# Kernel tuning notes

Hardware: AMD Instinct MI355X
Metric: run time of the kernel (lower is better)

Reference implementation:

```python
import jax, jax.numpy as jnp
import numpy as np

LOC_SIZE, TIM_SIZE = 50000, 48
LOC_EMB, TIM_EMB = 512, 32
IN = LOC_EMB + TIM_EMB  # 544
HID = 1024
SEQ, TGT = 4096, 1024


def _gru(x, Wih, Whh, bih, bhh):
    """PyTorch-convention GRU over [S, IN] -> [S, HID], h0 = 0."""
    gi = x @ Wih.T + bih  # [S, 3H] precomputed input gates
    H = Whh.shape[1]

    def step(h, gi_t):
        gh = Whh @ h + bhh
        i_r, i_z, i_n = jnp.split(gi_t, 3)
        h_r, h_z, h_n = jnp.split(gh, 3)
        r = jax.nn.sigmoid(i_r + h_r)
        z = jax.nn.sigmoid(i_z + h_z)
        n = jnp.tanh(i_n + r * h_n)
        h_new = (1.0 - z) * n + z * h
        return h_new, h_new

    _, hs = jax.lax.scan(step, jnp.zeros((H,), x.dtype), gi)
    return hs


def setup_inputs() -> dict:
    key = jax.random.key(0)
    ks = jax.random.split(key, 16)
    s = 0.02
    inp = {
        "loc": jax.random.randint(ks[0], (SEQ, 1), 0, LOC_SIZE),
        "tim": jax.random.randint(ks[1], (SEQ, 1), 0, TIM_SIZE),
        "target_len": TGT,
        "emb_loc": jax.random.normal(ks[2], (LOC_SIZE, LOC_EMB), jnp.float32) * s,
        "emb_tim": jax.random.normal(ks[3], (TIM_SIZE, TIM_EMB), jnp.float32) * s,
        "Wih_enc": jax.random.normal(ks[4], (3 * HID, IN), jnp.float32) * s,
        "Whh_enc": jax.random.normal(ks[5], (3 * HID, HID), jnp.float32) * s,
        "bih_enc": jnp.zeros((3 * HID,), jnp.float32),
        "bhh_enc": jnp.zeros((3 * HID,), jnp.float32),
        "Wih_dec": jax.random.normal(ks[6], (3 * HID, IN), jnp.float32) * s,
        "Whh_dec": jax.random.normal(ks[7], (3 * HID, HID), jnp.float32) * s,
        "bih_dec": jnp.zeros((3 * HID,), jnp.float32),
        "bhh_dec": jnp.zeros((3 * HID,), jnp.float32),
        "W_fc": jax.random.normal(ks[8], (LOC_SIZE, 2 * HID), jnp.float32) * s,
        "b_fc": jnp.zeros((LOC_SIZE,), jnp.float32),
    }
    return inp


def reference(loc, tim, target_len, emb_loc, emb_tim,
              Wih_enc, Whh_enc, bih_enc, bhh_enc,
              Wih_dec, Whh_dec, bih_dec, bhh_dec,
              W_fc, b_fc):
    # embeddings, batch dim of 1 squeezed: [S, IN]
    x = jnp.concatenate([emb_loc[loc[:, 0]], emb_tim[tim[:, 0]]], axis=1)
    # dropout is identity in eval mode
    hidden_history = _gru(x[:-target_len], Wih_enc, Whh_enc, bih_enc, bhh_enc)  # [S-T, H]
    hidden_state = _gru(x[-target_len:], Wih_dec, Whh_dec, bih_dec, bhh_dec)    # [T, H]
    # 'dot' attention: fused GEMM + row softmax (replaces the O(T*S) python loop)
    energies = hidden_state @ hidden_history.T                                   # [T, S-T]
    attn_weights = jax.nn.softmax(energies, axis=-1)
    context = attn_weights @ hidden_history                                      # [T, H]
    out = jnp.concatenate([hidden_state, context], axis=1)                       # [T, 2H]
    y = out @ W_fc.T + b_fc                                                      # [T, LOC_SIZE]
    return jax.nn.log_softmax(y, axis=-1)
```

## Files before the change

kernel.cpp:

```cpp
#include <hip/hip_runtime.h>
#include <hip/hip_bf16.h>
#include <cstdint>

typedef __attribute__((ext_vector_type(4))) float floatx4;
typedef __attribute__((ext_vector_type(8))) __bf16 bf16x8;
typedef __attribute__((ext_vector_type(4))) __bf16 bf16x4;
typedef unsigned long long u64t;

#define HID    1024
#define SEQ    4096
#define TGT    1024
#define ENC_T  3072
#define IN_DIM 544
#define NCLS   50000

__global__ __launch_bounds__(128) void embed_kernel(
    const int* __restrict__ loc, const int* __restrict__ tim,
    const float* __restrict__ el, const float* __restrict__ et,
    float* __restrict__ x) {
  int row = blockIdx.x, t = threadIdx.x;
  int li = loc[row], ti = tim[row];
  float4 v = *(const float4*)(el + (size_t)li * 512 + t * 4);
  *(float4*)(x + (size_t)row * IN_DIM + t * 4) = v;
  if (t < 8) {
    float4 w = *(const float4*)(et + (size_t)ti * 32 + t * 4);
    *(float4*)(x + (size_t)row * IN_DIM + 512 + t * 4) = w;
  }
}

#define BK  64
#define LDT 72

__global__ __launch_bounds__(256) void gemm_nt(
    const float* __restrict__ A, int lda,
    const float* __restrict__ B, int ldb,
    float* __restrict__ C, int ldc,
    const float* __restrict__ bias,
    int M, int N, int K) {
  __shared__ __bf16 As[128 * LDT];
  __shared__ __bf16 Bs[128 * LDT];
  const int tid = threadIdx.x;
  const int bm = blockIdx.x * 128, bn = blockIdx.y * 128;
  const int wave = tid >> 6, lane = tid & 63;
  const int wm = (wave & 1) * 64, wn = (wave >> 1) * 64;
  const int fr = lane & 15;
  const int kq = (lane >> 4) * 8;

  floatx4 acc[4][4];
#pragma unroll
  for (int i = 0; i < 4; i++)
#pragma unroll
    for (int j = 0; j < 4; j++) acc[i][j] = (floatx4){0.f, 0.f, 0.f, 0.f};

  const int nkt = (K + BK - 1) / BK;
  for (int kt = 0; kt < nkt; ++kt) {
    const int k0 = kt * BK;
#pragma unroll
    for (int i = 0; i < 8; i++) {
      int flat = tid + i * 256;
      int r = flat >> 4;
      int c4 = (flat & 15) * 4;
      float4 va = {0, 0, 0, 0}, vb = {0, 0, 0, 0};
      if (k0 + c4 < K) {
        va = *(const float4*)(A + (size_t)(bm + r) * lda + k0 + c4);
        if (bn + r < N) vb = *(const float4*)(B + (size_t)(bn + r) * ldb + k0 + c4);
      }
      *(bf16x4*)(As + r * LDT + c4) =
          (bf16x4){(__bf16)va.x, (__bf16)va.y, (__bf16)va.z, (__bf16)va.w};
      *(bf16x4*)(Bs + r * LDT + c4) =
          (bf16x4){(__bf16)vb.x, (__bf16)vb.y, (__bf16)vb.z, (__bf16)vb.w};
    }
    __syncthreads();
#pragma unroll
    for (int kh = 0; kh < 2; ++kh) {
      const int kf = kh * 32 + kq;
      bf16x8 af[4], bfr[4];
#pragma unroll
      for (int i = 0; i < 4; i++) {
        af[i]  = *(const bf16x8*)(As + (wm + i * 16 + fr) * LDT + kf);
        bfr[i] = *(const bf16x8*)(Bs + (wn + i * 16 + fr) * LDT + kf);
      }
#pragma unroll
      for (int mi = 0; mi < 4; mi++)
#pragma unroll
        for (int ni = 0; ni < 4; ni++)
          acc[mi][ni] = __builtin_amdgcn_mfma_f32_16x16x32_bf16(
              af[mi], bfr[ni], acc[mi][ni], 0, 0, 0);
    }
    __syncthreads();
  }

  const int em = (lane >> 4) * 4;
#pragma unroll
  for (int mi = 0; mi < 4; mi++) {
#pragma unroll
    for (int ni = 0; ni < 4; ni++) {
      int gn = bn + wn + ni * 16 + fr;
      if (gn < N) {
        float bv = bias ? bias[gn] : 0.f;
        int gm = bm + wm + mi * 16 + em;
#pragma unroll
        for (int r2 = 0; r2 < 4; r2++)
          C[(size_t)(gm + r2) * ldc + gn] = acc[mi][ni][r2] + bv;
      }
    }
  }
}

#define SC_WGS 128

__device__ __forceinline__ float bsel(unsigned int u, int half) {
  return __builtin_bit_cast(float, half ? (u & 0xffff0000u) : (u << 16));
}

__global__ __launch_bounds__(256) void scan_kernel(
    const float* __restrict__ Whh_e, const float* __restrict__ bhh_e, const float* __restrict__ gi_e,
    const float* __restrict__ Whh_d, const float* __restrict__ bhh_d, const float* __restrict__ gi_d,
    float* __restrict__ Hh, float* __restrict__ HhT, float* __restrict__ outcat,
    u64t* __restrict__ hbuf_e, u64t* __restrict__ hbuf_d) {
  const bool enc = blockIdx.x < SC_WGS;
  const int wid = enc ? blockIdx.x : (blockIdx.x - SC_WGS);
  const int T = enc ? ENC_T : TGT;
  const float* Whh = enc ? Whh_e : Whh_d;
  const float* bhh = enc ? bhh_e : bhh_d;
  const float* gi  = enc ? gi_e : gi_d;
  u64t* hbuf = enc ? hbuf_e : hbuf_d;

  __shared__ uint2 wrz[8 * 512];
  __shared__ unsigned int wnn[8 * 512];
  const int tid = threadIdx.x;

  for (int i = tid; i < 8 * 512; i += 256) {
    int el = i >> 9, k2 = i & 511;
    int rb = wid * 8 + el;
    float2 w0 = *(const float2*)(Whh + (size_t)(0 * HID + rb) * HID + 2 * k2);
    float2 w1 = *(const float2*)(Whh + (size_t)(1 * HID + rb) * HID + 2 * k2);
    float2 w2 = *(const float2*)(Whh + (size_t)(2 * HID + rb) * HID + 2 * k2);
    unsigned int p0 = (unsigned int)__builtin_bit_cast(unsigned short, (__bf16)w0.x) |
                      ((unsigned int)__builtin_bit_cast(unsigned short, (__bf16)w0.y) << 16);
    unsigned int p1 = (unsigned int)__builtin_bit_cast(unsigned short, (__bf16)w1.x) |
                      ((unsigned int)__builtin_bit_cast(unsigned short, (__bf16)w1.y) << 16);
    unsigned int p2 = (unsigned int)__builtin_bit_cast(unsigned short, (__bf16)w2.x) |
                      ((unsigned int)__builtin_bit_cast(unsigned short, (__bf16)w2.y) << 16);
    wrz[i] = make_uint2(p0, p1);
    wnn[i] = p2;
  }
  __syncthreads();

  const int l = tid & 63;
  const int w = tid >> 6;
  const int le0 = w * 2, le1 = le0 + 1;
  const int e0 = wid * 8 + le0;
  const int half = l & 1;
  const int kbase = l >> 1;

  float bq = 0.f;
  if (l < 3) bq = bhh[l * HID + e0];
  else if (l >= 4 && l < 7) bq = bhh[(l - 4) * HID + (e0 + 1)];

  long budget = 1L << 21;

  for (int t = 0; t < T; ++t) {
    float gval = 0.f;
    if (l < 3) gval = gi[(size_t)t * 3072 + l * HID + e0];
    else if (l >= 4 && l < 7) gval = gi[(size_t)t * 3072 + (l - 4) * HID + (e0 + 1)];

    const u64t* hp = hbuf + ((t + 1) & 1) * HID;
    float ar0, az0, an0, ar1, az1, an1, hpe = 0.f;
    for (;;) {
      u64t hv[16];
#pragma unroll
      for (int j = 0; j < 16; ++j)
        hv[j] = __hip_atomic_load(hp + l + 64 * j, __ATOMIC_RELAXED, __HIP_MEMORY_SCOPE_AGENT);
      u64t we = 0;
      if (l < 2) we = __hip_atomic_load(hp + e0 + l, __ATOMIC_RELAXED, __HIP_MEMORY_SCOPE_AGENT);
      bool ok = true;
      ar0 = az0 = an0 = ar1 = az1 = an1 = 0.f;
#pragma unroll
      for (int j = 0; j < 16; ++j) {
        ok &= (unsigned int)(hv[j] >> 32) >= (unsigned int)t;
        float h = __builtin_bit_cast(float, (unsigned int)hv[j]);
        int k2 = kbase + 32 * j;
        uint2 u0 = wrz[le0 * 512 + k2];
        unsigned int n0 = wnn[le0 * 512 + k2];
        uint2 u1 = wrz[le1 * 512 + k2];
        unsigned int n1 = wnn[le1 * 512 + k2];
        ar0 += bsel(u0.x, half) * h;
        az0 += bsel(u0.y, half) * h;
        an0 += bsel(n0, half) * h;
        ar1 += bsel(u1.x, half) * h;
        az1 += bsel(u1.y, half) * h;
        an1 += bsel(n1, half) * h;
      }
      if (l < 2) {
        ok &= (unsigned int)(we >> 32) >= (unsigned int)t;
        hpe = __builtin_bit_cast(float, (unsigned int)we);
      }
      if (__all(ok)) break;
      if (--budget < 0) break;
    }
#pragma unroll
    for (int o = 32; o; o >>= 1) {
      ar0 += __shfl_xor(ar0, o); az0 += __shfl_xor(az0, o); an0 += __shfl_xor(an0, o);
      ar1 += __shfl_xor(ar1, o); az1 += __shfl_xor(az1, o); an1 += __shfl_xor(an1, o);
    }
    int base = half * 4;
    float i_r = __shfl(gval, base + 0);
    float i_z = __shfl(gval, base + 1);
    float i_n = __shfl(gval, base + 2);
    float b_r = __shfl(bq, base + 0);
    float b_z = __shfl(bq, base + 1);
    float b_n = __shfl(bq, base + 2);
    __syncthreads();
    if (l < 2) {
      float sr = l ? ar1 : ar0;
      float sz = l ? az1 : az0;
      float sn = l ? an1 : an0;
      int e = e0 + l;
      float r = 1.f / (1.f + expf(-(i_r + sr + b_r)));
      float z = 1.f / (1.f + expf(-(i_z + sz + b_z)));
      float nn2 = tanhf(i_n + r * (sn + b_n));
      float hnew = (1.f - z) * nn2 + z * hpe;
      u64t pk = ((u64t)(unsigned int)(t + 1) << 32) |
                (u64t)__builtin_bit_cast(unsigned int, hnew);
      __hip_atomic_store(&hbuf[(t & 1) * HID + e], pk,
                         __ATOMIC_RELAXED, __HIP_MEMORY_SCOPE_AGENT);
      if (enc) {
        Hh[(size_t)t * HID + e] = hnew;
        HhT[(size_t)e * ENC_T + t] = hnew;
      } else {
        outcat[(size_t)t * 2048 + e] = hnew;
      }
    }
  }
}

__device__ __forceinline__ float wave_max(float v) {
#pragma unroll
  for (int o = 32; o; o >>= 1) v = fmaxf(v, __shfl_xor(v, o));
  return v;
}
__device__ __forceinline__ float wave_sum(float v) {
#pragma unroll
  for (int o = 32; o; o >>= 1) v += __shfl_xor(v, o);
  return v;
}

__global__ __launch_bounds__(256) void softmax_kernel(float* __restrict__ E) {
  __shared__ float red[4];
  int row = blockIdx.x;
  float* p = E + (size_t)row * ENC_T;
  int tid = threadIdx.x, wave = tid >> 6;
  float v[12];
  float m = -3.4e38f;
#pragma unroll
  for (int j = 0; j < 12; j++) { v[j] = p[tid + j * 256]; m = fmaxf(m, v[j]); }
  m = wave_max(m);
  if ((tid & 63) == 0) red[wave] = m;
  __syncthreads();
  m = fmaxf(fmaxf(red[0], red[1]), fmaxf(red[2], red[3]));
  __syncthreads();
  float s = 0.f;
#pragma unroll
  for (int j = 0; j < 12; j++) { v[j] = expf(v[j] - m); s += v[j]; }
  s = wave_sum(s);
  if ((tid & 63) == 0) red[wave] = s;
  __syncthreads();
  s = red[0] + red[1] + red[2] + red[3];
  float inv = 1.f / s;
#pragma unroll
  for (int j = 0; j < 12; j++) p[tid + j * 256] = v[j] * inv;
}

__global__ __launch_bounds__(256) void lse_kernel(const float* __restrict__ Y,
                                                  float* __restrict__ lse) {
  __shared__ float red[4];
  int row = blockIdx.x;
  const float* p = Y + (size_t)row * NCLS;
  int tid = threadIdx.x, wave = tid >> 6;
  float m = -3.4e38f;
  for (int c = tid; c < NCLS; c += 256) m = fmaxf(m, p[c]);
  m = wave_max(m);
  if ((tid & 63) == 0) red[wave] = m;
  __syncthreads();
  m = fmaxf(fmaxf(red[0], red[1]), fmaxf(red[2], red[3]));
  __syncthreads();
  float s = 0.f;
  for (int c = tid; c < NCLS; c += 256) s += expf(p[c] - m);
  s = wave_sum(s);
  if ((tid & 63) == 0) red[wave] = s;
  __syncthreads();
  if (tid == 0) lse[row] = m + logf(red[0] + red[1] + red[2] + red[3]);
}

__global__ __launch_bounds__(256) void sub_kernel(float* __restrict__ Y,
                                                  const float* __restrict__ lse) {
  const unsigned total = (unsigned)TGT * (NCLS / 4);
  unsigned stride = gridDim.x * 256;
  for (unsigned i = blockIdx.x * 256 + threadIdx.x; i < total; i += stride) {
    unsigned row = i / (NCLS / 4);
    float l = lse[row];
    float4 v = ((float4*)Y)[i];
    v.x -= l; v.y -= l; v.z -= l; v.w -= l;
    ((float4*)Y)[i] = v;
  }
}

extern "C" void kernel_launch(void* const* d_in, const int* in_sizes, int n_in,
                              void* d_out, int out_size, void* d_ws, size_t ws_size,
                              hipStream_t stream) {
  const int*   loc     = (const int*)d_in[0];
  const int*   tim     = (const int*)d_in[1];
  const float* emb_loc = (const float*)d_in[3];
  const float* emb_tim = (const float*)d_in[4];
  const float* Wih_e   = (const float*)d_in[5];
  const float* Whh_e   = (const float*)d_in[6];
  const float* bih_e   = (const float*)d_in[7];
  const float* bhh_e   = (const float*)d_in[8];
  const float* Wih_d   = (const float*)d_in[9];
  const float* Whh_d   = (const float*)d_in[10];
  const float* bih_d   = (const float*)d_in[11];
  const float* bhh_d   = (const float*)d_in[12];
  const float* W_fc    = (const float*)d_in[13];
  const float* b_fc    = (const float*)d_in[14];
  float* out = (float*)d_out;

  float* ws = (float*)d_ws;
  u64t* hbuf_e = (u64t*)ws;
  u64t* hbuf_d = (u64t*)(ws + 4096);
  float* lse    = ws + 8192;
  float* x      = ws + 9216;
  float* gi_e   = x + (size_t)SEQ * IN_DIM;
  float* gi_d   = gi_e + (size_t)ENC_T * 3072;
  float* Hh     = gi_d + (size_t)TGT * 3072;
  float* HhT    = Hh + (size_t)ENC_T * HID;
  float* outcat = HhT + (size_t)HID * ENC_T;
  float* energ  = outcat + (size_t)TGT * 2048;

  hipMemsetAsync(d_ws, 0, 8192 * sizeof(float), stream);

  embed_kernel<<<SEQ, 128, 0, stream>>>(loc, tim, emb_loc, emb_tim, x);

  gemm_nt<<<dim3(ENC_T / 128, 3072 / 128), 256, 0, stream>>>(
      x, IN_DIM, Wih_e, IN_DIM, gi_e, 3072, bih_e, ENC_T, 3072, IN_DIM);
  gemm_nt<<<dim3(TGT / 128, 3072 / 128), 256, 0, stream>>>(
      x + (size_t)ENC_T * IN_DIM, IN_DIM, Wih_d, IN_DIM, gi_d, 3072, bih_d, TGT, 3072, IN_DIM);

  scan_kernel<<<2 * SC_WGS, 256, 0, stream>>>(Whh_e, bhh_e, gi_e, Whh_d, bhh_d, gi_d,
                                              Hh, HhT, outcat, hbuf_e, hbuf_d);

  gemm_nt<<<dim3(TGT / 128, ENC_T / 128), 256, 0, stream>>>(
      outcat, 2048, Hh, HID, energ, ENC_T, nullptr, TGT, ENC_T, HID);
  softmax_kernel<<<TGT, 256, 0, stream>>>(energ);
  gemm_nt<<<dim3(TGT / 128, HID / 128), 256, 0, stream>>>(
      energ, ENC_T, HhT, ENC_T, outcat + HID, 2048, nullptr, TGT, HID, ENC_T);

  gemm_nt<<<dim3(TGT / 128, (NCLS + 127) / 128), 256, 0, stream>>>(
      outcat, 2048, W_fc, 2048, out, NCLS, b_fc, TGT, NCLS, 2048);

  lse_kernel<<<TGT, 256, 0, stream>>>(out, lse);
  sub_kernel<<<4096, 256, 0, stream>>>(out, lse);
}
```

Before: 15.11 ms.

## Pack GRU hidden-state exchange as bf16 value plus 16-bit step tag

The cross-workgroup hidden-state buffer now stores each element as a 32-bit word: a bf16 value plus a 16-bit step counter, replacing the 64-bit fp32-plus-tag word. Each lane polls half as many 64-bit atomic words per step, and each word carries two h elements. Each workgroup keeps its own previous h in an fp32 register instead of re-reading it, and the per-step __syncthreads is dropped. The cost is that the recurrent matvec now uses a bf16-rounded h, which may cost accuracy over the long scan.

```diff
diff --git a/kernel.cpp b/kernel.cpp
--- a/kernel.cpp
+++ b/kernel.cpp
@@ -109,22 +109,25 @@
 
 #define SC_WGS 128
 
-__device__ __forceinline__ float bsel(unsigned int u, int half) {
-  return __builtin_bit_cast(float, half ? (u & 0xffff0000u) : (u << 16));
+__device__ __forceinline__ float flo(unsigned int u) {
+  return __builtin_bit_cast(float, u << 16);
+}
+__device__ __forceinline__ float fhi(unsigned int u) {
+  return __builtin_bit_cast(float, u & 0xffff0000u);
 }
 
 __global__ __launch_bounds__(256) void scan_kernel(
     const float* __restrict__ Whh_e, const float* __restrict__ bhh_e, const float* __restrict__ gi_e,
     const float* __restrict__ Whh_d, const float* __restrict__ bhh_d, const float* __restrict__ gi_d,
     float* __restrict__ Hh, float* __restrict__ HhT, float* __restrict__ outcat,
-    u64t* __restrict__ hbuf_e, u64t* __restrict__ hbuf_d) {
+    unsigned int* __restrict__ hbuf_e, unsigned int* __restrict__ hbuf_d) {
   const bool enc = blockIdx.x < SC_WGS;
   const int wid = enc ? blockIdx.x : (blockIdx.x - SC_WGS);
   const int T = enc ? ENC_T : TGT;
   const float* Whh = enc ? Whh_e : Whh_d;
   const float* bhh = enc ? bhh_e : bhh_d;
   const float* gi  = enc ? gi_e : gi_d;
-  u64t* hbuf = enc ? hbuf_e : hbuf_d;
+  unsigned int* hbuf = enc ? hbuf_e : hbuf_d;
 
   __shared__ uint2 wrz[8 * 512];
   __shared__ unsigned int wnn[8 * 512];
@@ -151,13 +154,17 @@
   const int w = tid >> 6;
   const int le0 = w * 2, le1 = le0 + 1;
   const int e0 = wid * 8 + le0;
-  const int half = l & 1;
-  const int kbase = l >> 1;
 
   float bq = 0.f;
   if (l < 3) bq = bhh[l * HID + e0];
   else if (l >= 4 && l < 7) bq = bhh[(l - 4) * HID + (e0 + 1)];
 
+  const uint2* wrz0 = wrz + le0 * 512;
+  const uint2* wrz1 = wrz + le1 * 512;
+  const unsigned int* wnn0 = wnn + le0 * 512;
+  const unsigned int* wnn1 = wnn + le1 * 512;
+
+  float h_own = 0.f;
   long budget = 1L << 21;
 
   for (int t = 0; t < T; ++t) {
@@ -165,36 +172,34 @@
     if (l < 3) gval = gi[(size_t)t * 3072 + l * HID + e0];
     else if (l >= 4 && l < 7) gval = gi[(size_t)t * 3072 + (l - 4) * HID + (e0 + 1)];
 
-    const u64t* hp = hbuf + ((t + 1) & 1) * HID;
-    float ar0, az0, an0, ar1, az1, an1, hpe = 0.f;
+    const u64t* hp = (const u64t*)(hbuf + ((t + 1) & 1) * HID);
+    const unsigned int tlo = (unsigned int)t;
+    float ar0, az0, an0, ar1, az1, an1;
     for (;;) {
-      u64t hv[16];
-#pragma unroll
-      for (int j = 0; j < 16; ++j)
+      u64t hv[8];
+#pragma unroll
+      for (int j = 0; j < 8; ++j)
         hv[j] = __hip_atomic_load(hp + l + 64 * j, __ATOMIC_RELAXED, __HIP_MEMORY_SCOPE_AGENT);
-      u64t we = 0;
-      if (l < 2) we = __hip_atomic_load(hp + e0 + l, __ATOMIC_RELAXED, __HIP_MEMORY_SCOPE_AGENT);
       bool ok = true;
       ar0 = az0 = an0 = ar1 = az1 = an1 = 0.f;
 #pragma unroll
-      for (int j = 0; j < 16; ++j) {
-        ok &= (unsigned int)(hv[j] >> 32) >= (unsigned int)t;
-        float h = __builtin_bit_cast(float, (unsigned int)hv[j]);
-        int k2 = kbase + 32 * j;
-        uint2 u0 = wrz[le0 * 512 + k2];
-        unsigned int n0 = wnn[le0 * 512 + k2];
-        uint2 u1 = wrz[le1 * 512 + k2];
-        unsigned int n1 = wnn[le1 * 512 + k2];
-        ar0 += bsel(u0.x, half) * h;
-        az0 += bsel(u0.y, half) * h;
-        an0 += bsel(n0, half) * h;
-        ar1 += bsel(u1.x, half) * h;
-        az1 += bsel(u1.y, half) * h;
-        an1 += bsel(n1, half) * h;
-      }
-      if (l < 2) {
-        ok &= (unsigned int)(we >> 32) >= (unsigned int)t;
-        hpe = __builtin_bit_cast(float, (unsigned int)we);
+      for (int j = 0; j < 8; ++j) {
+        unsigned int w0 = (unsigned int)hv[j];
+        unsigned int w1 = (unsigned int)(hv[j] >> 32);
+        ok &= ((w0 >> 16) >= tlo) & ((w1 >> 16) >= tlo);
+        float h0 = flo(w0);
+        float h1 = flo(w1);
+        int i = l + 64 * j;
+        uint2 u0 = wrz0[i];
+        unsigned int n0 = wnn0[i];
+        uint2 u1 = wrz1[i];
+        unsigned int n1 = wnn1[i];
+        ar0 += flo(u0.x) * h0 + fhi(u0.x) * h1;
+        az0 += flo(u0.y) * h0 + fhi(u0.y) * h1;
+        an0 += flo(n0) * h0 + fhi(n0) * h1;
+        ar1 += flo(u1.x) * h0 + fhi(u1.x) * h1;
+        az1 += flo(u1.y) * h0 + fhi(u1.y) * h1;
+        an1 += flo(n1) * h0 + fhi(n1) * h1;
       }
       if (__all(ok)) break;
       if (--budget < 0) break;
@@ -204,14 +209,13 @@
       ar0 += __shfl_xor(ar0, o); az0 += __shfl_xor(az0, o); an0 += __shfl_xor(an0, o);
       ar1 += __shfl_xor(ar1, o); az1 += __shfl_xor(az1, o); an1 += __shfl_xor(an1, o);
     }
-    int base = half * 4;
+    int base = (l & 1) * 4;
     float i_r = __shfl(gval, base + 0);
     float i_z = __shfl(gval, base + 1);
     float i_n = __shfl(gval, base + 2);
     float b_r = __shfl(bq, base + 0);
     float b_z = __shfl(bq, base + 1);
     float b_n = __shfl(bq, base + 2);
-    __syncthreads();
     if (l < 2) {
       float sr = l ? ar1 : ar0;
       float sz = l ? az1 : az0;
@@ -220,9 +224,10 @@
       float r = 1.f / (1.f + expf(-(i_r + sr + b_r)));
       float z = 1.f / (1.f + expf(-(i_z + sz + b_z)));
       float nn2 = tanhf(i_n + r * (sn + b_n));
-      float hnew = (1.f - z) * nn2 + z * hpe;
-      u64t pk = ((u64t)(unsigned int)(t + 1) << 32) |
-                (u64t)__builtin_bit_cast(unsigned int, hnew);
+      float hnew = (1.f - z) * nn2 + z * h_own;
+      h_own = hnew;
+      unsigned int pk = ((unsigned int)(t + 1) << 16) |
+                        (unsigned int)__builtin_bit_cast(unsigned short, (__bf16)hnew);
       __hip_atomic_store(&hbuf[(t & 1) * HID + e], pk,
                          __ATOMIC_RELAXED, __HIP_MEMORY_SCOPE_AGENT);
       if (enc) {
@@ -326,10 +331,10 @@
   float* out = (float*)d_out;
 
   float* ws = (float*)d_ws;
-  u64t* hbuf_e = (u64t*)ws;
-  u64t* hbuf_d = (u64t*)(ws + 4096);
-  float* lse    = ws + 8192;
-  float* x      = ws + 9216;
+  unsigned int* hbuf_e = (unsigned int*)ws;
+  unsigned int* hbuf_d = (unsigned int*)(ws + 2048);
+  float* lse    = ws + 4096;
+  float* x      = ws + 5120;
   float* gi_e   = x + (size_t)SEQ * IN_DIM;
   float* gi_d   = gi_e + (size_t)ENC_T * 3072;
   float* Hh     = gi_d + (size_t)TGT * 3072;
@@ -337,7 +342,7 @@
   float* outcat = HhT + (size_t)HID * ENC_T;
   float* energ  = outcat + (size_t)TGT * 2048;
 
-  hipMemsetAsync(d_ws, 0, 8192 * sizeof(float), stream);
+  hipMemsetAsync(d_ws, 0, 4096 * sizeof(float), stream);
 
   embed_kernel<<<SEQ, 128, 0, stream>>>(loc, tim, emb_loc, emb_tim, x);
 
```

Measured after the change: 16.99 ms. 1.12x slower.
